# Kernel optimization log

Measured on AMD Instinct MI355X. Metric: run time of the kernel, lower is better.

## Reference

```python
import jax, jax.numpy as jnp
import numpy as np

N_QUBITS = 8
N_LAYERS = 3
N_FEATURES = 16
BATCH = 65536
DIM = 2 ** N_QUBITS  # 256 amplitudes
EPS = 1e-5  # torch BatchNorm1d default eps

# Precompute CNOT permutations (wire 0 = most significant bit, PennyLane order)
_idx = np.arange(DIM)
CNOT_PERMS = []
for _i in range(N_QUBITS):
    for _j in range(_i + 1, N_QUBITS):
        _c = (_idx >> (N_QUBITS - 1 - _i)) & 1
        CNOT_PERMS.append(np.where(_c == 1, _idx ^ (1 << (N_QUBITS - 1 - _j)), _idx))
# PauliZ sign table: (DIM, N_QUBITS), +1 for bit 0, -1 for bit 1
Z_SIGNS = np.stack([1.0 - 2.0 * ((_idx >> (N_QUBITS - 1 - i)) & 1) for i in range(N_QUBITS)], axis=1).astype(np.float32)


def _ry(theta):
    t = jnp.asarray(theta)
    c = jnp.cos(t / 2).astype(jnp.complex64)
    s = jnp.sin(t / 2).astype(jnp.complex64)
    return jnp.stack([jnp.stack([c, -s], -1), jnp.stack([s, c], -1)], -2)


def _rx(theta):
    t = jnp.asarray(theta)
    c = jnp.cos(t / 2).astype(jnp.complex64)
    s = (-1j) * jnp.sin(t / 2).astype(jnp.complex64)
    return jnp.stack([jnp.stack([c, s], -1), jnp.stack([s, c], -1)], -2)


def _rz(theta):
    e = jnp.exp(-0.5j * jnp.asarray(theta, jnp.complex64))
    z = jnp.zeros_like(e)
    return jnp.stack([jnp.stack([e, z], -1), jnp.stack([z, jnp.conj(e)], -1)], -2)


def _apply_1q(state, U, w):
    # state: (B, DIM); U: (2,2) shared or (B,2,2) per-sample; wire w
    B = state.shape[0]
    left, right = 2 ** w, 2 ** (N_QUBITS - 1 - w)
    s = state.reshape(B, left, 2, right)
    if U.ndim == 2:
        out = jnp.einsum('st,bpsq->bptq', U, s)
    else:
        out = jnp.einsum('bst,bpsq->bptq', U, s)
    return out.reshape(B, DIM)


def _quantum(angles, qw):
    # Batched state-vector simulation of the PennyLane circuit.
    # angles: (B, N_QUBITS) float32 encoding angles; qw: (N_LAYERS, N_QUBITS, 3)
    B = angles.shape[0]
    state = jnp.zeros((B, DIM), jnp.complex64).at[:, 0].set(1.0 + 0.0j)
    for i in range(N_QUBITS):  # RY(inputs[i]) encoding, per-sample angles
        state = _apply_1q(state, _ry(angles[:, i]), i)
    for l in range(N_LAYERS):
        for i in range(N_QUBITS):
            state = _apply_1q(state, _rx(qw[l, i, 0]), i)
            state = _apply_1q(state, _ry(qw[l, i, 1]), i)
            state = _apply_1q(state, _rz(qw[l, i, 2]), i)
        for perm in CNOT_PERMS:  # all-pairs CNOT(i, j), i < j
            state = state[:, perm]
    probs = state.real ** 2 + state.imag ** 2  # (B, DIM)
    return probs @ jnp.asarray(Z_SIGNS)  # (B, N_QUBITS) <Z_i> expectations


def _bn(h, g, b, m, v):
    # BatchNorm1d in inference mode (running stats)
    return (h - m) * jax.lax.rsqrt(v + EPS) * g + b


def _forward(x, W1, b1, g1, bt1, m1, v1, W2, b2, g2, bt2, m2, v2, W3, b3, q_weights, W4, b4, g4, bt4, m4, v4, W5, b5, W6, b6):
    h = jax.nn.relu(_bn(x @ W1.T + b1, g1, bt1, m1, v1))
    h = jax.nn.relu(_bn(h @ W2.T + b2, g2, bt2, m2, v2))
    pre = jnp.tanh(h @ W3.T + b3)  # (B, N_QUBITS)
    # Original detaches before the quantum circuit -> no grad through it
    q_out = _quantum(jax.lax.stop_gradient(pre), jax.lax.stop_gradient(q_weights))
    h = jax.nn.relu(_bn(q_out @ W4.T + b4, g4, bt4, m4, v4))
    h = jax.nn.relu(h @ W5.T + b5)
    return h @ W6.T + b6  # (B, 1)


def setup_inputs() -> dict:
    key = jax.random.key(0)
    ks = jax.random.split(key, 8)

    def lin(k, o, i):
        return (jax.random.normal(k, (o, i), jnp.float32) / np.sqrt(i)).astype(jnp.float32)

    return {
        'x': jax.random.normal(ks[0], (BATCH, N_FEATURES), jnp.float32),
        'W1': lin(ks[1], 128, N_FEATURES), 'b1': jnp.zeros((128,), jnp.float32),
        'g1': jnp.ones((128,), jnp.float32), 'bt1': jnp.zeros((128,), jnp.float32),
        'm1': jnp.zeros((128,), jnp.float32), 'v1': jnp.ones((128,), jnp.float32),
        'W2': lin(ks[2], 64, 128), 'b2': jnp.zeros((64,), jnp.float32),
        'g2': jnp.ones((64,), jnp.float32), 'bt2': jnp.zeros((64,), jnp.float32),
        'm2': jnp.zeros((64,), jnp.float32), 'v2': jnp.ones((64,), jnp.float32),
        'W3': lin(ks[3], N_QUBITS, 64), 'b3': jnp.zeros((N_QUBITS,), jnp.float32),
        'q_weights': jax.random.normal(ks[4], (N_LAYERS, N_QUBITS, 3), jnp.float32) * 0.1,
        'W4': lin(ks[5], 32, N_QUBITS), 'b4': jnp.zeros((32,), jnp.float32),
        'g4': jnp.ones((32,), jnp.float32), 'bt4': jnp.zeros((32,), jnp.float32),
        'm4': jnp.zeros((32,), jnp.float32), 'v4': jnp.ones((32,), jnp.float32),
        'W5': lin(ks[6], 16, 32), 'b5': jnp.zeros((16,), jnp.float32),
        'W6': lin(ks[7], 1, 16), 'b6': jnp.zeros((1,), jnp.float32),
    }


def reference(x, W1, b1, g1, bt1, m1, v1, W2, b2, g2, bt2, m2, v2, W3, b3, q_weights, W4, b4, g4, bt4, m4, v4, W5, b5, W6, b6):
    return _forward(x, W1, b1, g1, bt1, m1, v1, W2, b2, g2, bt2, m2, v2, W3, b3, q_weights, W4, b4, g4, bt4, m4, v4, W5, b5, W6, b6)
```

## Files before the change

kernel.cpp:

```cpp
#include <hip/hip_runtime.h>

__device__ __forceinline__ float2 cmul(float2 a, float2 b){
    return make_float2(a.x*b.x - a.y*b.y, a.x*b.y + a.y*b.x);
}
__device__ __forceinline__ float2 cadd(float2 a, float2 b){
    return make_float2(a.x + b.x, a.y + b.y);
}
__device__ __forceinline__ unsigned short f2h(float f){
    _Float16 h = (_Float16)f;
    return __builtin_bit_cast(unsigned short, h);
}

typedef _Float16 f16x8 __attribute__((ext_vector_type(8)));
typedef float    f32x4 __attribute__((ext_vector_type(4)));

__device__ __forceinline__ void split8(const float* p, f16x8& ah, f16x8& al){
    const f32x4* q = (const f32x4*)p;
    f32x4 v0 = q[0], v1 = q[1];
    float av[8] = {v0[0],v0[1],v0[2],v0[3],v1[0],v1[1],v1[2],v1[3]};
    #pragma unroll
    for (int j=0;j<8;++j){
        _Float16 h = (_Float16)av[j];
        ah[j] = h;
        al[j] = (_Float16)(av[j] - (float)h);
    }
}

__device__ __forceinline__ void build_gates(const float* qw, int l, int c, float2 (*G)[2][2]){
    if (c < 8){
        int i = c;
        float t0 = 0.5f*qw[l*24 + i*3 + 0];
        float t1 = 0.5f*qw[l*24 + i*3 + 1];
        float t2 = 0.5f*qw[l*24 + i*3 + 2];
        float c1,s1,c2,s2,c3,s3;
        sincosf(t0,&s1,&c1); sincosf(t1,&s2,&c2); sincosf(t2,&s3,&c3);
        float2 RX[2][2] = {{{c1,0.f},{0.f,-s1}},{{0.f,-s1},{c1,0.f}}};
        float2 RY[2][2] = {{{c2,0.f},{s2,0.f}},{{-s2,0.f},{c2,0.f}}};
        float2 M[2][2];
        #pragma unroll
        for (int r=0;r<2;++r)
            #pragma unroll
            for (int cc=0;cc<2;++cc)
                M[r][cc] = cadd(cmul(RY[r][0],RX[0][cc]), cmul(RY[r][1],RX[1][cc]));
        float2 e  = {c3,-s3};
        float2 ec = {c3, s3};
        G[i][0][0]=cmul(e, M[0][0]); G[i][0][1]=cmul(e, M[0][1]);
        G[i][1][0]=cmul(ec,M[1][0]); G[i][1][1]=cmul(ec,M[1][1]);
    }
}
__device__ __forceinline__ int cnot_perm(int k){
    int r = k;
    for (int i=6;i>=0;--i)
        for (int j=7;j>i;--j)
            if ((r >> (7-i)) & 1) r ^= 1 << (7-j);
    return r;
}

__global__ void k_build_prep(const float* __restrict__ qw, float2* __restrict__ U,
                       const float* __restrict__ W1, const float* __restrict__ b1,
                       const float* __restrict__ g1, const float* __restrict__ bt1,
                       const float* __restrict__ m1, const float* __restrict__ v1,
                       const float* __restrict__ W2, const float* __restrict__ b2,
                       const float* __restrict__ g2, const float* __restrict__ bt2,
                       const float* __restrict__ m2, const float* __restrict__ v2,
                       const float* __restrict__ W3,
                       unsigned short* __restrict__ H1w, float* __restrict__ c1,
                       unsigned short* __restrict__ H2w, float* __restrict__ c2,
                       unsigned short* __restrict__ H3w){
    if (blockIdx.y == 2){
        if (blockIdx.x >= 8) return;
        int tid = blockIdx.x*256 + threadIdx.x;
        const int stride = 8*256;
        for (int i=tid; i<4096; i+=stride){ int n=i>>5, k=i&31;
            float s=g1[n]*rsqrtf(v1[n]+1e-5f);
            H1w[i] = f2h(k<16 ? W1[n*16+k]*s : 0.f); }
        for (int i=tid; i<128;  i+=stride){ float s=g1[i]*rsqrtf(v1[i]+1e-5f); c1[i]=(b1[i]-m1[i])*s+bt1[i]; }
        for (int i=tid; i<8192; i+=stride){ int n=i>>7;
            float s=g2[n]*rsqrtf(v2[n]+1e-5f);
            H2w[i] = f2h(W2[i]*s); }
        for (int i=tid; i<64;   i+=stride){ float s=g2[i]*rsqrtf(v2[i]+1e-5f); c2[i]=(b2[i]-m2[i])*s+bt2[i]; }
        for (int i=tid; i<1024; i+=stride){ int n=i>>6, k=i&63;
            H3w[i] = f2h(n<8 ? W3[n*64+k] : 0.f); }
        return;
    }
    __shared__ float2 G[8][2][2];
    int l = blockIdx.y, k = blockIdx.x, c = threadIdx.x;
    build_gates(qw, l, c, G);
    __syncthreads();
    int r = cnot_perm(k);
    float2 p = {1.f, 0.f};
    #pragma unroll
    for (int i=0;i<8;++i)
        p = cmul(p, G[i][(r>>(7-i))&1][(c>>(7-i))&1]);
    U[l*65536 + k*256 + c] = p;
}

__global__ __launch_bounds__(256) void k_rowmm(const float* __restrict__ qw,
                                              const float2* __restrict__ U,
                                              unsigned short* __restrict__ WqS){
    __shared__ float2 G[8][2][2];
    __shared__ float2 vs[256];
    __shared__ float2 ws[256];
    int r = blockIdx.x, c = threadIdx.x;
    build_gates(qw, 2, c, G);
    __syncthreads();
    int pr = cnot_perm(r);
    float2 p = {1.f, 0.f};
    #pragma unroll
    for (int i=0;i<8;++i)
        p = cmul(p, G[i][(pr>>(7-i))&1][(c>>(7-i))&1]);
    vs[c] = p;
    __syncthreads();
    float2 acc = {0.f,0.f};
    #pragma unroll 8
    for (int m=0;m<256;++m)
        acc = cadd(acc, cmul(vs[m], U[65536 + m*256 + c]));
    ws[c] = acc;
    __syncthreads();
    float2 z = {0.f,0.f};
    #pragma unroll 8
    for (int m=0;m<256;++m)
        z = cadd(z, cmul(ws[m], U[m*256 + c]));
    int T = r >> 4, l15 = r & 15;
    int ks = c >> 5, lq = (c >> 3) & 3, j = c & 7;
    int lane = lq*16 + l15;
    WqS[((T     *8 + ks)*64 + lane)*8 + j] = f2h(z.x);
    WqS[(((T+16)*8 + ks)*64 + lane)*8 + j] = f2h(z.y);
}

#define A_STRIDE 264
#define P_STRIDE 269
__global__ __launch_bounds__(256,2) void k_fused(
    const float* __restrict__ x,
    const unsigned short* __restrict__ H1w, const float* __restrict__ c1,
    const unsigned short* __restrict__ H2w, const float* __restrict__ c2,
    const unsigned short* __restrict__ H3w, const float* __restrict__ b3,
    const unsigned short* __restrict__ WqS,
    const float* __restrict__ W4, const float* __restrict__ b4, const float* __restrict__ g4,
    const float* __restrict__ bt4, const float* __restrict__ m4, const float* __restrict__ v4,
    const float* __restrict__ W5, const float* __restrict__ b5,
    const float* __restrict__ W6, const float* __restrict__ b6,
    float* __restrict__ out)
{
    __shared__ __align__(16) char smem[45952];
    unsigned short* H1 = (unsigned short*)smem;
    unsigned short* H2 = (unsigned short*)(smem + 17408);
    float* XS   = (float*)(smem + 26624);
    float* preL = (float*)(smem + 35840);
    unsigned short* As = (unsigned short*)smem;
    float* probs = (float*)smem;
    float* qacc  = (float*)(smem + 34432);
    float* qout  = (float*)(smem + 43648);

    int tid = threadIdx.x;
    int row0 = blockIdx.x*64;
    int wave = tid>>6, lane = tid&63, l15 = lane&15, lq = lane>>4;
    const f32x4 zz = {0.f,0.f,0.f,0.f};

    {
        int r = tid >> 2, q = tid & 3;
        const float4* xp = (const float4*)(x + (row0 + r)*16 + q*4);
        float4 v = xp[0];
        *(float4*)(XS + r*36 + q*4) = v;
        *(float4*)(XS + r*36 + 16 + q*4) = make_float4(0.f,0.f,0.f,0.f);
    }
    __syncthreads();

    {
        f32x4 acc1[4][2];
        #pragma unroll
        for (int mt=0;mt<4;++mt){ acc1[mt][0]=zz; acc1[mt][1]=zz; }
        #pragma unroll
        for (int mt=0; mt<4; ++mt){
            f16x8 ah, al;
            split8(XS + (mt*16+l15)*36 + lq*8, ah, al);
            #pragma unroll
            for (int t=0;t<2;++t){
                int nt = wave + t*4;
                f16x8 b = *(const f16x8*)(H1w + (nt*16+l15)*32 + lq*8);
                acc1[mt][t] = __builtin_amdgcn_mfma_f32_16x16x32_f16(ah, b, acc1[mt][t], 0,0,0);
                acc1[mt][t] = __builtin_amdgcn_mfma_f32_16x16x32_f16(al, b, acc1[mt][t], 0,0,0);
            }
        }
        #pragma unroll
        for (int t=0;t<2;++t){
            int n = (wave + t*4)*16 + l15;
            float bias = c1[n];
            #pragma unroll
            for (int mt=0; mt<4; ++mt)
                #pragma unroll
                for (int reg=0; reg<4; ++reg){
                    int rowl = mt*16 + lq*4 + reg;
                    H1[rowl*136 + n] = f2h(fmaxf(acc1[mt][t][reg] + bias, 0.f));
                }
        }
    }
    __syncthreads();

    {
        f32x4 acc2[4];
        #pragma unroll
        for (int mt=0;mt<4;++mt) acc2[mt]=zz;
        #pragma unroll
        for (int ks=0; ks<4; ++ks){
            f16x8 b = *(const f16x8*)(H2w + (wave*16+l15)*128 + ks*32 + lq*8);
            #pragma unroll
            for (int mt=0; mt<4; ++mt){
                f16x8 a = *(const f16x8*)(H1 + (mt*16+l15)*136 + ks*32 + lq*8);
                acc2[mt] = __builtin_amdgcn_mfma_f32_16x16x32_f16(a, b, acc2[mt], 0,0,0);
            }
        }
        int n = wave*16 + l15;
        float bias = c2[n];
        #pragma unroll
        for (int mt=0; mt<4; ++mt)
            #pragma unroll
            for (int reg=0; reg<4; ++reg){
                int rowl = mt*16 + lq*4 + reg;
                H2[rowl*72 + n] = f2h(fmaxf(acc2[mt][reg] + bias, 0.f));
            }
    }
    __syncthreads();

    {
        f32x4 acc3 = zz;
        #pragma unroll
        for (int ks=0; ks<2; ++ks){
            f16x8 b = *(const f16x8*)(H3w + l15*64 + ks*32 + lq*8);
            f16x8 a = *(const f16x8*)(H2 + (wave*16+l15)*72 + ks*32 + lq*8);
            acc3 = __builtin_amdgcn_mfma_f32_16x16x32_f16(a, b, acc3, 0,0,0);
        }
        if (l15 < 8){
            float bias = b3[l15];
            #pragma unroll
            for (int reg=0; reg<4; ++reg){
                int rowl = wave*16 + lq*4 + reg;
                preL[rowl*8 + l15] = tanhf(acc3[reg] + bias);
            }
        }
    }
    __syncthreads();

    {
        int row = tid & 63, q = tid >> 6;
        const float4* p4 = (const float4*)(preL + row*8);
        float4 pa = p4[0], pb = p4[1];
        float th[8] = {pa.x,pa.y,pa.z,pa.w,pb.x,pb.y,pb.z,pb.w};
        float cs[8], sn[8];
        #pragma unroll
        for (int i=0;i<8;++i){ __sincosf(0.5f*th[i], &sn[i], &cs[i]); sn[i] = -sn[i]; }
        float F = (q&2 ? sn[0] : cs[0]) * (q&1 ? sn[1] : cs[1]);
        float Pm[8], Pl[8];
        #pragma unroll
        for (int a2=0;a2<8;++a2){
            Pm[a2] = (a2&4?sn[2]:cs[2]) * (a2&2?sn[3]:cs[3]) * (a2&1?sn[4]:cs[4]);
            Pl[a2] = (a2&4?sn[5]:cs[5]) * (a2&2?sn[6]:cs[6]) * (a2&1?sn[7]:cs[7]);
        }
        unsigned short* arow = As + row*A_STRIDE + q*64;
        #pragma unroll
        for (int mh=0;mh<8;++mh){
            float fm = F * Pm[mh];
            uint4 w;
            w.x = (unsigned)f2h(fm*Pl[0]) | ((unsigned)f2h(fm*Pl[1])<<16);
            w.y = (unsigned)f2h(fm*Pl[2]) | ((unsigned)f2h(fm*Pl[3])<<16);
            w.z = (unsigned)f2h(fm*Pl[4]) | ((unsigned)f2h(fm*Pl[5])<<16);
            w.w = (unsigned)f2h(fm*Pl[6]) | ((unsigned)f2h(fm*Pl[7])<<16);
            *reinterpret_cast<uint4*>(arow + mh*8) = w;
        }
    }
    __syncthreads();

    const f16x8* Bp[8];
    #pragma unroll
    for (int t=0;t<8;++t){
        int T = ((t>>2)<<4) + wave*4 + (t&3);
        Bp[t] = reinterpret_cast<const f16x8*>(WqS + T*4096) + lane;
    }
    const f16x8* Ap[4];
    #pragma unroll
    for (int mt=0;mt<4;++mt)
        Ap[mt] = reinterpret_cast<const f16x8*>(As + (mt*16 + l15)*A_STRIDE + lq*8);

    f32x4 acc[4][8];
    #pragma unroll
    for (int mt=0;mt<4;++mt)
        #pragma unroll
        for (int t=0;t<8;++t) acc[mt][t] = zz;

    f16x8 bfr[2][8];
    #pragma unroll
    for (int t=0;t<8;++t) bfr[0][t] = Bp[t][0];

    #pragma unroll
    for (int ks=0;ks<8;++ks){
        int cur = ks & 1;
        if (ks < 7){
            #pragma unroll
            for (int t=0;t<8;++t) bfr[cur^1][t] = Bp[t][(ks+1)*64];
        }
        f16x8 afr[4];
        #pragma unroll
        for (int mt=0;mt<4;++mt) afr[mt] = Ap[mt][ks*4];
        #pragma unroll
        for (int mt=0;mt<4;++mt)
            #pragma unroll
            for (int t=0;t<8;++t)
                acc[mt][t] = __builtin_amdgcn_mfma_f32_16x16x32_f16(afr[mt], bfr[cur][t], acc[mt][t], 0, 0, 0);
    }
    __syncthreads();

    #pragma unroll
    for (int h=0; h<2; ++h){
        #pragma unroll
        for (int mtl=0; mtl<2; ++mtl){
            int mt = h*2 + mtl;
            #pragma unroll
            for (int t=0;t<4;++t){
                #pragma unroll
                for (int reg=0;reg<4;++reg){
                    float sr = acc[mt][t][reg];
                    float si = acc[mt][t+4][reg];
                    int prow = mtl*16 + lq*4 + reg;
                    int pcol = wave*64 + t*16 + l15;
                    probs[prow*P_STRIDE + pcol] = fmaf(sr,sr,si*si);
                }
            }
        }
        __syncthreads();
        {
            int row = tid & 31, q = tid >> 5;
            const float* pb = probs + row*P_STRIDE + q*32;
            float S=0.f,z3=0.f,z4=0.f,z5=0.f,z6=0.f,z7=0.f;
            #pragma unroll
            for (int j=0;j<32;++j){
                float p = pb[j];
                S  += p;
                z3 += (j&16)? -p : p;
                z4 += (j&8) ? -p : p;
                z5 += (j&4) ? -p : p;
                z6 += (j&2) ? -p : p;
                z7 += (j&1) ? -p : p;
            }
            float* qa = qacc + (q*32 + row)*9;
            qa[0] = (q&4)? -S : S;
            qa[1] = (q&2)? -S : S;
            qa[2] = (q&1)? -S : S;
            qa[3] = z3; qa[4] = z4; qa[5] = z5; qa[6] = z6; qa[7] = z7;
        }
        __syncthreads();
        {
            int r = tid >> 3, i = tid & 7;
            float v = 0.f;
            #pragma unroll
            for (int g=0; g<8; ++g) v += qacc[(g*32 + r)*9 + i];
            qout[(h*32 + r)*9 + i] = v;
        }
    }
    __syncthreads();

    if (tid < 64){
        int r = tid;
        float qv[8];
        #pragma unroll
        for (int i=0;i<8;++i) qv[i] = qout[r*9+i];
        float h4[32];
        #pragma unroll
        for (int j=0;j<32;++j){
            float a = b4[j];
            #pragma unroll
            for (int i=0;i<8;++i) a = fmaf(qv[i], W4[j*8+i], a);
            float sc = g4[j]*rsqrtf(v4[j]+1e-5f);
            a = fmaf(a - m4[j], sc, bt4[j]);
            h4[j] = fmaxf(a, 0.f);
        }
        float h5[16];
        #pragma unroll
        for (int j=0;j<16;++j){
            float a = b5[j];
            #pragma unroll
            for (int k=0;k<32;++k) a = fmaf(h4[k], W5[j*32+k], a);
            h5[j] = fmaxf(a, 0.f);
        }
        float o = b6[0];
        #pragma unroll
        for (int k=0;k<16;++k) o = fmaf(h5[k], W6[k], o);
        out[blockIdx.x*64 + r] = o;
    }
}

extern "C" void kernel_launch(void* const* d_in, const int* in_sizes, int n_in,
                              void* d_out, int out_size, void* d_ws, size_t ws_size,
                              hipStream_t stream) {
    (void)in_sizes; (void)n_in; (void)out_size; (void)ws_size;
    const float* x   = (const float*)d_in[0];
    const float* W1  = (const float*)d_in[1];
    const float* b1  = (const float*)d_in[2];
    const float* g1  = (const float*)d_in[3];
    const float* bt1 = (const float*)d_in[4];
    const float* m1  = (const float*)d_in[5];
    const float* v1  = (const float*)d_in[6];
    const float* W2  = (const float*)d_in[7];
    const float* b2  = (const float*)d_in[8];
    const float* g2  = (const float*)d_in[9];
    const float* bt2 = (const float*)d_in[10];
    const float* m2  = (const float*)d_in[11];
    const float* v2  = (const float*)d_in[12];
    const float* W3  = (const float*)d_in[13];
    const float* b3  = (const float*)d_in[14];
    const float* qw  = (const float*)d_in[15];
    const float* W4  = (const float*)d_in[16];
    const float* b4  = (const float*)d_in[17];
    const float* g4  = (const float*)d_in[18];
    const float* bt4 = (const float*)d_in[19];
    const float* m4  = (const float*)d_in[20];
    const float* v4  = (const float*)d_in[21];
    const float* W5  = (const float*)d_in[22];
    const float* b5  = (const float*)d_in[23];
    const float* W6  = (const float*)d_in[24];
    const float* b6  = (const float*)d_in[25];

    char* ws = (char*)d_ws;
    float2* U   = (float2*)ws;
    unsigned short* WqS = (unsigned short*)(U + 2*65536);
    unsigned short* H1w = WqS + 512*256;
    unsigned short* H2w = H1w + 4096;
    unsigned short* H3w = H2w + 8192;
    float* c1 = (float*)(H3w + 1024);
    float* c2 = c1 + 128;

    k_build_prep<<<dim3(256,3), 256, 0, stream>>>(qw, U,
                                  W1,b1,g1,bt1,m1,v1, W2,b2,g2,bt2,m2,v2, W3,
                                  H1w,c1,H2w,c2,H3w);
    k_rowmm<<<256, 256, 0, stream>>>(qw, U, WqS);
    k_fused<<<1024, 256, 0, stream>>>(x, H1w,c1, H2w,c2, H3w,b3, WqS,
                                      W4,b4,g4,bt4,m4,v4, W5,b5,W6,b6,
                                      (float*)d_out);
}
```

Before: 174.4 us.

## Halve rows per block, split-fp16 hidden layers, parallelize classical tail MLP

The fused kernel now handles 32 rows per block instead of 64 and launches twice as many blocks. Register accumulators shrink and the two-pass probability reduction becomes a single pass. The H1/H2 activations are stored as hi/lo fp16 pairs with doubled MFMAs for accuracy. The final MLP is spread across all 256 threads through shared memory instead of 64 threads doing it serially. The intent is to raise occupancy and reduce the serial tail, at the cost of reloading the WqS B-operand from global memory twice as often and doing more MFMAs in the early layers.

```diff
diff --git a/kernel.cpp b/kernel.cpp
--- a/kernel.cpp
+++ b/kernel.cpp
@@ -142,36 +142,42 @@
     const float* __restrict__ W6, const float* __restrict__ b6,
     float* __restrict__ out)
 {
-    __shared__ __align__(16) char smem[45952];
-    unsigned short* H1 = (unsigned short*)smem;
-    unsigned short* H2 = (unsigned short*)(smem + 17408);
+    __shared__ __align__(16) char smem[44800];
+    unsigned short* H1h = (unsigned short*)smem;
+    unsigned short* H1l = (unsigned short*)(smem + 8704);
+    unsigned short* H2h = (unsigned short*)(smem + 17408);
+    unsigned short* H2l = (unsigned short*)(smem + 22016);
     float* XS   = (float*)(smem + 26624);
-    float* preL = (float*)(smem + 35840);
+    float* preL = (float*)(smem + 31232);
     unsigned short* As = (unsigned short*)smem;
     float* probs = (float*)smem;
     float* qacc  = (float*)(smem + 34432);
     float* qout  = (float*)(smem + 43648);
+    float* h4b   = (float*)smem;
+    float* h5b   = (float*)(smem + 4224);
 
     int tid = threadIdx.x;
-    int row0 = blockIdx.x*64;
+    int row0 = blockIdx.x*32;
     int wave = tid>>6, lane = tid&63, l15 = lane&15, lq = lane>>4;
     const f32x4 zz = {0.f,0.f,0.f,0.f};
 
-    {
+    if (tid < 128){
         int r = tid >> 2, q = tid & 3;
         const float4* xp = (const float4*)(x + (row0 + r)*16 + q*4);
-        float4 v = xp[0];
-        *(float4*)(XS + r*36 + q*4) = v;
+        *(float4*)(XS + r*36 + q*4) = xp[0];
+    } else {
+        int t2 = tid - 128;
+        int r = t2 >> 2, q = t2 & 3;
         *(float4*)(XS + r*36 + 16 + q*4) = make_float4(0.f,0.f,0.f,0.f);
     }
     __syncthreads();
 
     {
-        f32x4 acc1[4][2];
-        #pragma unroll
-        for (int mt=0;mt<4;++mt){ acc1[mt][0]=zz; acc1[mt][1]=zz; }
-        #pragma unroll
-        for (int mt=0; mt<4; ++mt){
+        f32x4 acc1[2][2];
+        #pragma unroll
+        for (int mt=0;mt<2;++mt){ acc1[mt][0]=zz; acc1[mt][1]=zz; }
+        #pragma unroll
+        for (int mt=0; mt<2; ++mt){
             f16x8 ah, al;
             split8(XS + (mt*16+l15)*36 + lq*8, ah, al);
             #pragma unroll
@@ -187,48 +193,57 @@
             int n = (wave + t*4)*16 + l15;
             float bias = c1[n];
             #pragma unroll
-            for (int mt=0; mt<4; ++mt)
+            for (int mt=0; mt<2; ++mt)
                 #pragma unroll
                 for (int reg=0; reg<4; ++reg){
                     int rowl = mt*16 + lq*4 + reg;
-                    H1[rowl*136 + n] = f2h(fmaxf(acc1[mt][t][reg] + bias, 0.f));
+                    float a = fmaxf(acc1[mt][t][reg] + bias, 0.f);
+                    _Float16 h = (_Float16)a;
+                    H1h[rowl*136 + n] = __builtin_bit_cast(unsigned short, h);
+                    H1l[rowl*136 + n] = f2h(a - (float)h);
                 }
         }
     }
     __syncthreads();
 
     {
-        f32x4 acc2[4];
-        #pragma unroll
-        for (int mt=0;mt<4;++mt) acc2[mt]=zz;
+        f32x4 acc2[2];
+        acc2[0]=zz; acc2[1]=zz;
         #pragma unroll
         for (int ks=0; ks<4; ++ks){
             f16x8 b = *(const f16x8*)(H2w + (wave*16+l15)*128 + ks*32 + lq*8);
             #pragma unroll
-            for (int mt=0; mt<4; ++mt){
-                f16x8 a = *(const f16x8*)(H1 + (mt*16+l15)*136 + ks*32 + lq*8);
-                acc2[mt] = __builtin_amdgcn_mfma_f32_16x16x32_f16(a, b, acc2[mt], 0,0,0);
+            for (int mt=0; mt<2; ++mt){
+                f16x8 ah = *(const f16x8*)(H1h + (mt*16+l15)*136 + ks*32 + lq*8);
+                f16x8 al = *(const f16x8*)(H1l + (mt*16+l15)*136 + ks*32 + lq*8);
+                acc2[mt] = __builtin_amdgcn_mfma_f32_16x16x32_f16(ah, b, acc2[mt], 0,0,0);
+                acc2[mt] = __builtin_amdgcn_mfma_f32_16x16x32_f16(al, b, acc2[mt], 0,0,0);
             }
         }
         int n = wave*16 + l15;
         float bias = c2[n];
         #pragma unroll
-        for (int mt=0; mt<4; ++mt)
+        for (int mt=0; mt<2; ++mt)
             #pragma unroll
             for (int reg=0; reg<4; ++reg){
                 int rowl = mt*16 + lq*4 + reg;
-                H2[rowl*72 + n] = f2h(fmaxf(acc2[mt][reg] + bias, 0.f));
+                float a = fmaxf(acc2[mt][reg] + bias, 0.f);
+                _Float16 h = (_Float16)a;
+                H2h[rowl*72 + n] = __builtin_bit_cast(unsigned short, h);
+                H2l[rowl*72 + n] = f2h(a - (float)h);
             }
     }
     __syncthreads();
 
-    {
+    if (wave < 2){
         f32x4 acc3 = zz;
         #pragma unroll
         for (int ks=0; ks<2; ++ks){
             f16x8 b = *(const f16x8*)(H3w + l15*64 + ks*32 + lq*8);
-            f16x8 a = *(const f16x8*)(H2 + (wave*16+l15)*72 + ks*32 + lq*8);
-            acc3 = __builtin_amdgcn_mfma_f32_16x16x32_f16(a, b, acc3, 0,0,0);
+            f16x8 ah = *(const f16x8*)(H2h + (wave*16+l15)*72 + ks*32 + lq*8);
+            f16x8 al = *(const f16x8*)(H2l + (wave*16+l15)*72 + ks*32 + lq*8);
+            acc3 = __builtin_amdgcn_mfma_f32_16x16x32_f16(ah, b, acc3, 0,0,0);
+            acc3 = __builtin_amdgcn_mfma_f32_16x16x32_f16(al, b, acc3, 0,0,0);
         }
         if (l15 < 8){
             float bias = b3[l15];
@@ -242,23 +257,24 @@
     __syncthreads();
 
     {
-        int row = tid & 63, q = tid >> 6;
+        int row = tid & 31, q = tid >> 5;
         const float4* p4 = (const float4*)(preL + row*8);
         float4 pa = p4[0], pb = p4[1];
         float th[8] = {pa.x,pa.y,pa.z,pa.w,pb.x,pb.y,pb.z,pb.w};
         float cs[8], sn[8];
         #pragma unroll
         for (int i=0;i<8;++i){ __sincosf(0.5f*th[i], &sn[i], &cs[i]); sn[i] = -sn[i]; }
-        float F = (q&2 ? sn[0] : cs[0]) * (q&1 ? sn[1] : cs[1]);
-        float Pm[8], Pl[8];
-        #pragma unroll
-        for (int a2=0;a2<8;++a2){
-            Pm[a2] = (a2&4?sn[2]:cs[2]) * (a2&2?sn[3]:cs[3]) * (a2&1?sn[4]:cs[4]);
+        float F = (q&4 ? sn[0] : cs[0]) * (q&2 ? sn[1] : cs[1]) * (q&1 ? sn[2] : cs[2]);
+        float Pm[4], Pl[8];
+        #pragma unroll
+        for (int a2=0;a2<4;++a2)
+            Pm[a2] = (a2&2?sn[3]:cs[3]) * (a2&1?sn[4]:cs[4]);
+        #pragma unroll
+        for (int a2=0;a2<8;++a2)
             Pl[a2] = (a2&4?sn[5]:cs[5]) * (a2&2?sn[6]:cs[6]) * (a2&1?sn[7]:cs[7]);
-        }
-        unsigned short* arow = As + row*A_STRIDE + q*64;
-        #pragma unroll
-        for (int mh=0;mh<8;++mh){
+        unsigned short* arow = As + row*A_STRIDE + q*32;
+        #pragma unroll
+        for (int mh=0;mh<4;++mh){
             float fm = F * Pm[mh];
             uint4 w;
             w.x = (unsigned)f2h(fm*Pl[0]) | ((unsigned)f2h(fm*Pl[1])<<16);
@@ -276,14 +292,14 @@
         int T = ((t>>2)<<4) + wave*4 + (t&3);
         Bp[t] = reinterpret_cast<const f16x8*>(WqS + T*4096) + lane;
     }
-    const f16x8* Ap[4];
-    #pragma unroll
-    for (int mt=0;mt<4;++mt)
+    const f16x8* Ap[2];
+    #pragma unroll
+    for (int mt=0;mt<2;++mt)
         Ap[mt] = reinterpret_cast<const f16x8*>(As + (mt*16 + l15)*A_STRIDE + lq*8);
 
-    f32x4 acc[4][8];
-    #pragma unroll
-    for (int mt=0;mt<4;++mt)
+    f32x4 acc[2][8];
+    #pragma unroll
+    for (int mt=0;mt<2;++mt)
         #pragma unroll
         for (int t=0;t<8;++t) acc[mt][t] = zz;
 
@@ -298,11 +314,11 @@
             #pragma unroll
             for (int t=0;t<8;++t) bfr[cur^1][t] = Bp[t][(ks+1)*64];
         }
-        f16x8 afr[4];
-        #pragma unroll
-        for (int mt=0;mt<4;++mt) afr[mt] = Ap[mt][ks*4];
-        #pragma unroll
-        for (int mt=0;mt<4;++mt)
+        f16x8 afr[2];
+        #pragma unroll
+        for (int mt=0;mt<2;++mt) afr[mt] = Ap[mt][ks*4];
+        #pragma unroll
+        for (int mt=0;mt<2;++mt)
             #pragma unroll
             for (int t=0;t<8;++t)
                 acc[mt][t] = __builtin_amdgcn_mfma_f32_16x16x32_f16(afr[mt], bfr[cur][t], acc[mt][t], 0, 0, 0);
@@ -310,81 +326,85 @@
     __syncthreads();
 
     #pragma unroll
-    for (int h=0; h<2; ++h){
-        #pragma unroll
-        for (int mtl=0; mtl<2; ++mtl){
-            int mt = h*2 + mtl;
-            #pragma unroll
-            for (int t=0;t<4;++t){
-                #pragma unroll
-                for (int reg=0;reg<4;++reg){
-                    float sr = acc[mt][t][reg];
-                    float si = acc[mt][t+4][reg];
-                    int prow = mtl*16 + lq*4 + reg;
-                    int pcol = wave*64 + t*16 + l15;
-                    probs[prow*P_STRIDE + pcol] = fmaf(sr,sr,si*si);
-                }
+    for (int mt=0; mt<2; ++mt){
+        #pragma unroll
+        for (int t=0;t<4;++t){
+            #pragma unroll
+            for (int reg=0;reg<4;++reg){
+                float sr = acc[mt][t][reg];
+                float si = acc[mt][t+4][reg];
+                int prow = mt*16 + lq*4 + reg;
+                int pcol = wave*64 + t*16 + l15;
+                probs[prow*P_STRIDE + pcol] = fmaf(sr,sr,si*si);
             }
         }
-        __syncthreads();
-        {
-            int row = tid & 31, q = tid >> 5;
-            const float* pb = probs + row*P_STRIDE + q*32;
-            float S=0.f,z3=0.f,z4=0.f,z5=0.f,z6=0.f,z7=0.f;
-            #pragma unroll
-            for (int j=0;j<32;++j){
-                float p = pb[j];
-                S  += p;
-                z3 += (j&16)? -p : p;
-                z4 += (j&8) ? -p : p;
-                z5 += (j&4) ? -p : p;
-                z6 += (j&2) ? -p : p;
-                z7 += (j&1) ? -p : p;
-            }
-            float* qa = qacc + (q*32 + row)*9;
-            qa[0] = (q&4)? -S : S;
-            qa[1] = (q&2)? -S : S;
-            qa[2] = (q&1)? -S : S;
-            qa[3] = z3; qa[4] = z4; qa[5] = z5; qa[6] = z6; qa[7] = z7;
-        }
-        __syncthreads();
-        {
-            int r = tid >> 3, i = tid & 7;
-            float v = 0.f;
-            #pragma unroll
-            for (int g=0; g<8; ++g) v += qacc[(g*32 + r)*9 + i];
-            qout[(h*32 + r)*9 + i] = v;
-        }
-    }
-    __syncthreads();
-
-    if (tid < 64){
-        int r = tid;
+    }
+    __syncthreads();
+
+    {
+        int row = tid & 31, q = tid >> 5;
+        const float* pb = probs + row*P_STRIDE + q*32;
+        float S=0.f,z3=0.f,z4=0.f,z5=0.f,z6=0.f,z7=0.f;
+        #pragma unroll
+        for (int j=0;j<32;++j){
+            float p = pb[j];
+            S  += p;
+            z3 += (j&16)? -p : p;
+            z4 += (j&8) ? -p : p;
+            z5 += (j&4) ? -p : p;
+            z6 += (j&2) ? -p : p;
+            z7 += (j&1) ? -p : p;
+        }
+        float* qa = qacc + tid*9;
+        qa[0] = (q&4)? -S : S;
+        qa[1] = (q&2)? -S : S;
+        qa[2] = (q&1)? -S : S;
+        qa[3] = z3; qa[4] = z4; qa[5] = z5; qa[6] = z6; qa[7] = z7;
+    }
+    __syncthreads();
+    {
+        int r = tid >> 3, i = tid & 7;
+        float v = 0.f;
+        #pragma unroll
+        for (int g=0; g<8; ++g) v += qacc[(g*32 + r)*9 + i];
+        qout[r*9 + i] = v;
+    }
+    __syncthreads();
+
+    {
+        int row = tid & 31, s = tid >> 5;
         float qv[8];
         #pragma unroll
-        for (int i=0;i<8;++i) qv[i] = qout[r*9+i];
-        float h4[32];
-        #pragma unroll
-        for (int j=0;j<32;++j){
+        for (int i=0;i<8;++i) qv[i] = qout[row*9+i];
+        #pragma unroll
+        for (int jj=0;jj<4;++jj){
+            int j = s*4 + jj;
             float a = b4[j];
             #pragma unroll
             for (int i=0;i<8;++i) a = fmaf(qv[i], W4[j*8+i], a);
             float sc = g4[j]*rsqrtf(v4[j]+1e-5f);
             a = fmaf(a - m4[j], sc, bt4[j]);
-            h4[j] = fmaxf(a, 0.f);
-        }
-        float h5[16];
-        #pragma unroll
-        for (int j=0;j<16;++j){
+            h4b[row*33 + j] = fmaxf(a, 0.f);
+        }
+    }
+    __syncthreads();
+    {
+        int row = tid & 31, s = tid >> 5;
+        #pragma unroll
+        for (int jj=0;jj<2;++jj){
+            int j = s*2 + jj;
             float a = b5[j];
             #pragma unroll
-            for (int k=0;k<32;++k) a = fmaf(h4[k], W5[j*32+k], a);
-            h5[j] = fmaxf(a, 0.f);
-        }
+            for (int k=0;k<32;++k) a = fmaf(h4b[row*33+k], W5[j*32+k], a);
+            h5b[row*17 + j] = fmaxf(a, 0.f);
+        }
+    }
+    __syncthreads();
+    if (tid < 32){
         float o = b6[0];
         #pragma unroll
-        for (int k=0;k<16;++k) o = fmaf(h5[k], W6[k], o);
-        out[blockIdx.x*64 + r] = o;
+        for (int k=0;k<16;++k) o = fmaf(h5b[tid*17+k], W6[k], o);
+        out[row0 + tid] = o;
     }
 }
 
@@ -432,7 +452,7 @@
                                   W1,b1,g1,bt1,m1,v1, W2,b2,g2,bt2,m2,v2, W3,
                                   H1w,c1,H2w,c2,H3w);
     k_rowmm<<<256, 256, 0, stream>>>(qw, U, WqS);
-    k_fused<<<1024, 256, 0, stream>>>(x, H1w,c1, H2w,c2, H3w,b3, WqS,
+    k_fused<<<2048, 256, 0, stream>>>(x, H1w,c1, H2w,c2, H3w,b3, WqS,
                                       W4,b4,g4,bt4,m4,v4, W5,b5,W6,b6,
                                       (float*)d_out);
 }
```

New measurement: 176.8 us. About the same (+1.4%).
